# Performance work log

Measured on AMD Instinct MI355X. Metric: run time of the kernel, lower is better.

Reference implementation:

```python
import jax, jax.numpy as jnp
import numpy as np
from jax import lax

DIM = 256
NUM_HEADS = 8
SW = 7
HEAD_DIM = DIM // NUM_HEADS
SCALE = HEAD_DIM ** -0.5


def setup_inputs() -> dict:
    key = jax.random.key(0)
    ks = jax.random.split(key, 7)
    B, C, H, W = 8, DIM, 56, 56
    x = jax.random.normal(ks[0], (B, C, H, W), dtype=jnp.float32)
    w_qkv = jax.random.normal(ks[1], (3 * C, C), dtype=jnp.float32) * 0.02
    b_qkv = jnp.zeros((3 * C,), dtype=jnp.float32)
    # depthwise 3x3 kernel, OIHW with feature_group_count=C -> (C,1,3,3)
    w_dw = jax.random.normal(ks[2], (C, 1, 3, 3), dtype=jnp.float32) * 0.02
    b_dw = jnp.zeros((C,), dtype=jnp.float32)
    w_proj = jax.random.normal(ks[3], (C, C), dtype=jnp.float32) * 0.02
    b_proj = jnp.zeros((C,), dtype=jnp.float32)
    return {"x": x, "w_qkv": w_qkv, "b_qkv": b_qkv, "w_dw": w_dw,
            "b_dw": b_dw, "w_proj": w_proj, "b_proj": b_proj}


def _conv1x1(x, w, b):
    # x:[B,C,H,W], w:[O,C] -> [B,O,H,W]
    return jnp.einsum('bchw,oc->bohw', x, w) + b[None, :, None, None]


def _dwconv3x3(x, w, b):
    C = x.shape[1]
    y = lax.conv_general_dilated(x, w, window_strides=(1, 1), padding='SAME',
                                 dimension_numbers=('NCHW', 'OIHW', 'NCHW'),
                                 feature_group_count=C)
    return y + b[None, :, None, None]


def _stripe_attn_H(q, k, v, sw):
    # q,k,v: [B,h,C,H,W]; local attention within sw-thick horizontal stripes
    B, h, C, H, W = q.shape
    sw = min(sw, H)
    pad = (-H) % sw
    if pad:
        pw = [(0, 0)] * 3 + [(0, pad), (0, 0)]
        q = jnp.pad(q, pw); k = jnp.pad(k, pw); v = jnp.pad(v, pw)
    Hp = H + pad
    n = Hp // sw

    def rs(t):
        # -> [B,h,n, sw*W, C]
        return t.reshape(B, h, C, n, sw, W).transpose(0, 1, 3, 4, 5, 2).reshape(B, h, n, sw * W, C)

    qs, ks_, vs = rs(q) * SCALE, rs(k), rs(v)
    attn = jax.nn.softmax(jnp.einsum('bhnqc,bhnkc->bhnqk', qs, ks_), axis=-1)
    out = jnp.einsum('bhnqk,bhnkc->bhnqc', attn, vs)
    out = out.reshape(B, h, n, sw, W, C).transpose(0, 1, 5, 2, 3, 4).reshape(B, h, C, Hp, W)
    return out[:, :, :, :H, :]


def _stripe_attn_W(q, k, v, sw):
    # attention within sw-thick vertical stripes; softmax is permutation-
    # equivariant over the stripe sequence, so transposing H<->W and reusing
    # the H-stripe kernel computes identical math.
    t = lambda a: a.transpose(0, 1, 2, 4, 3)
    return t(_stripe_attn_H(t(q), t(k), t(v), sw))


def reference(x, w_qkv, b_qkv, w_dw, b_dw, w_proj, b_proj):
    B, C, H, W = x.shape
    hh = NUM_HEADS // 2
    qkv = _conv1x1(x, w_qkv, b_qkv)
    q, k, v = jnp.split(qkv, 3, axis=1)
    v = v + _dwconv3x3(v, w_dw, b_dw)

    def heads(t):
        return t.reshape(B, NUM_HEADS, HEAD_DIM, H, W)

    q, k, v = heads(q), heads(k), heads(v)
    out_h = _stripe_attn_H(q[:, :hh], k[:, :hh], v[:, :hh], SW)
    out_w = _stripe_attn_W(q[:, hh:], k[:, hh:], v[:, hh:], SW)
    out = jnp.concatenate([out_h, out_w], axis=1).reshape(B, C, H, W)
    return _conv1x1(out, w_proj, b_proj)
```

## Files before the change

### kernel.cpp

```cpp
#include <hip/hip_runtime.h>
#include <hip/hip_bf16.h>
#include <stdint.h>

#define Bn 8
#define Cn 256
#define Hn 56
#define Wn 56
#define HWn 3136
#define NHEADS 8
#define HDIM 32
#define SEQ 392
#define NSTR 8
#define QKV_LD 768
#define KSC (0.17677669529663689f * 1.4426950408889634f)

#if __has_builtin(__builtin_amdgcn_exp2f)
#define EXP2(x) __builtin_amdgcn_exp2f(x)
#else
#define EXP2(x) exp2f(x)
#endif

typedef short short8 __attribute__((ext_vector_type(8)));
typedef float floatx4 __attribute__((ext_vector_type(4)));

__device__ __forceinline__ unsigned short f2bf(float f) {
  union { float f; uint32_t u; } v; v.f = f;
  uint32_t u = v.u;
  u += 0x7fffu + ((u >> 16) & 1u);
  return (unsigned short)(u >> 16);
}
__device__ __forceinline__ float bf2f(unsigned short h) {
  union { uint32_t u; float f; } v; v.u = ((uint32_t)h) << 16;
  return v.f;
}
__device__ __forceinline__ uint32_t cvt_pk_bf16(float lo, float hi) {
  uint32_t r;
  asm("v_cvt_pk_bf16_f32 %0, %1, %2" : "=v"(r) : "v"(lo), "v"(hi));
  return r;
}
__device__ __forceinline__ void gload16(const unsigned short* g, unsigned short* l) {
  __builtin_amdgcn_global_load_lds((const __attribute__((address_space(1))) void*)g,
                                   (__attribute__((address_space(3))) void*)l, 16, 0, 0);
}

__global__ __launch_bounds__(256) void k_cvt2(const float* __restrict__ a,
                                              const float* __restrict__ b2,
                                              unsigned short* __restrict__ da,
                                              unsigned short* __restrict__ db) {
  int i = blockIdx.x * 256 + threadIdx.x;
  if (i < 49152) {
    float4 v = ((const float4*)a)[i];
    ushort4 o;
    o.x = f2bf(v.x); o.y = f2bf(v.y); o.z = f2bf(v.z); o.w = f2bf(v.w);
    ((ushort4*)da)[i] = o;
  } else {
    int k = i - 49152;
    float4 v = ((const float4*)b2)[k];
    ushort4 o;
    o.x = f2bf(v.x); o.y = f2bf(v.y); o.z = f2bf(v.z); o.w = f2bf(v.w);
    ((ushort4*)db)[k] = o;
  }
}

__global__ __launch_bounds__(256) void k_trans_x(const float* __restrict__ x,
                                                 unsigned short* __restrict__ xt) {
  __shared__ float tile[32][33];
  int pb = blockIdx.x, cb = blockIdx.y, b = blockIdx.z;
  int t = threadIdx.x;
  int c = t >> 3, p4 = (t & 7) * 4;
  float4 v = *(const float4*)(x + (((size_t)b * Cn + cb * 32 + c) * HWn + pb * 32 + p4));
  tile[c][p4 + 0] = v.x; tile[c][p4 + 1] = v.y; tile[c][p4 + 2] = v.z; tile[c][p4 + 3] = v.w;
  __syncthreads();
  int p = t >> 3, c4 = (t & 7) * 4;
  ushort4 o;
  o.x = f2bf(tile[c4 + 0][p]); o.y = f2bf(tile[c4 + 1][p]);
  o.z = f2bf(tile[c4 + 2][p]); o.w = f2bf(tile[c4 + 3][p]);
  *(ushort4*)(xt + (((size_t)b * HWn + pb * 32 + p) * Cn + cb * 32 + c4)) = o;
}

template <int EPI>
__global__ __launch_bounds__(512) void k_gemm(const unsigned short* __restrict__ A,
                                              const unsigned short* __restrict__ Bt,
                                              const float* __restrict__ bias,
                                              unsigned short* __restrict__ outB,
                                              float* __restrict__ outF,
                                              int M, int N, int K, int nm, int nper) {
  __shared__ __align__(16) char SH[EPI ? 67584 : 65536];
  unsigned short* As = (unsigned short*)SH;
  unsigned short* Bs = As + 16384;
  int t = threadIdx.x;
  int raw = blockIdx.x;
  int chunk = gridDim.x >> 3;
  int wg = (raw & 7) * chunk + (raw >> 3);
  int b = wg / nper, r = wg % nper;
  int m0 = (r % nm) * 128, n0 = (r / nm) * 128;
  const unsigned short* Bb = Bt + (size_t)b * N * K;
  int lane = t & 63, w = t >> 6;
  int wr = w >> 1, wc = w & 1;
  int g = lane >> 4, q = lane & 15;
  int srow8 = lane >> 3;
  int slot = lane & 7;

  const unsigned short* Ag[2];
  const unsigned short* Bg[2];
  bool bok[2];
  int ldst[2];
#pragma unroll
  for (int i = 0; i < 2; i++) {
    int row = i * 64 + w * 8 + srow8;
    int cs = slot ^ srow8;
    Ag[i] = A + (size_t)(m0 + row) * K + cs * 8;
    int nr = n0 + row;
    bok[i] = (nr < N);
    Bg[i] = Bb + (size_t)(bok[i] ? nr : (N - 1)) * K + cs * 8;
    ldst[i] = (i * 64 + w * 8) * 64;
  }

  floatx4 z4 = {0.f, 0.f, 0.f, 0.f};
  floatx4 acc[2][4];
#pragma unroll
  for (int i = 0; i < 2; i++)
#pragma unroll
    for (int j = 0; j < 4; j++) acc[i][j] = z4;

#pragma unroll
  for (int i = 0; i < 2; i++) gload16(Ag[i], &As[ldst[i]]);
#pragma unroll
  for (int i = 0; i < 2; i++) if (bok[i]) gload16(Bg[i], &Bs[ldst[i]]);
  asm volatile("s_waitcnt vmcnt(0)" ::: "memory");
  __syncthreads();

  int cur = 0;
  for (int tt = 0; tt < 4; tt++) {
    if (tt < 3) {
      int k0 = (tt + 1) * 64;
      int nb = (cur ^ 1) * 8192;
#pragma unroll
      for (int i = 0; i < 2; i++) gload16(Ag[i] + k0, &As[nb + ldst[i]]);
#pragma unroll
      for (int i = 0; i < 2; i++) if (bok[i]) gload16(Bg[i] + k0, &Bs[nb + ldst[i]]);
    }
    int cb = cur * 8192;
#pragma unroll
    for (int kk = 0; kk < 64; kk += 32) {
      short8 af[2], bfr[4];
#pragma unroll
      for (int i = 0; i < 2; i++) {
        int row = wr * 32 + i * 16 + q;
        af[i] = *(const short8*)&As[cb + row * 64 + ((((kk >> 3) + g) ^ (q & 7)) << 3)];
      }
#pragma unroll
      for (int j = 0; j < 4; j++) {
        int row = wc * 64 + j * 16 + q;
        bfr[j] = *(const short8*)&Bs[cb + row * 64 + ((((kk >> 3) + g) ^ (q & 7)) << 3)];
      }
#pragma unroll
      for (int i = 0; i < 2; i++)
#pragma unroll
        for (int j = 0; j < 4; j++)
          acc[i][j] = __builtin_amdgcn_mfma_f32_16x16x32_bf16(af[i], bfr[j], acc[i][j], 0, 0, 0);
    }
    if (tt < 3) {
      asm volatile("s_waitcnt vmcnt(0)" ::: "memory");
      __syncthreads();
      cur ^= 1;
    }
  }

  __syncthreads();
  if (EPI == 0) {
    unsigned short* E = (unsigned short*)SH;
#pragma unroll
    for (int i = 0; i < 2; i++) {
      int ob = m0 + wr * 32 + i * 16 + g * 4;
      float bs0 = bias[ob + 0], bs1 = bias[ob + 1], bs2 = bias[ob + 2], bs3 = bias[ob + 3];
      float sc = (ob >= 256 && ob < 512) ? KSC : 1.0f;
      int lobg = wr * 4 + i * 2 + (g >> 1);
#pragma unroll
      for (int j = 0; j < 4; j++) {
        int lc = wc * 64 + j * 16 + q;
        ushort4 o;
        o.x = f2bf((acc[i][j][0] + bs0) * sc);
        o.y = f2bf((acc[i][j][1] + bs1) * sc);
        o.z = f2bf((acc[i][j][2] + bs2) * sc);
        o.w = f2bf((acc[i][j][3] + bs3) * sc);
        *(ushort4*)&E[lc * 128 + ((lobg ^ (lc & 7)) << 3) + (g & 1) * 4] = o;
      }
    }
    __syncthreads();
    int c = t >> 2, part = t & 3;
    int col = n0 + c;
    if (col < N) {
      unsigned short* dst = outB + ((size_t)b * N + col) * M + m0;
#pragma unroll
      for (int k2 = part * 4; k2 < part * 4 + 4; k2++) {
        short8 v = *(const short8*)&E[c * 128 + ((k2 ^ (c & 7)) << 3)];
        *(short8*)(dst + k2 * 8) = v;
      }
    }
  } else {
    float* Ef = (float*)SH;
#pragma unroll
    for (int i = 0; i < 2; i++) {
      int ob = m0 + wr * 32 + i * 16 + g * 4;
      int lob = wr * 32 + i * 16 + g * 4;
      float bs0 = bias[ob + 0], bs1 = bias[ob + 1], bs2 = bias[ob + 2], bs3 = bias[ob + 3];
#pragma unroll
      for (int j = 0; j < 4; j++) {
        int lc = wc * 64 + j * 16 + q;
        Ef[(lob + 0) * 132 + lc] = acc[i][j][0] + bs0;
        Ef[(lob + 1) * 132 + lc] = acc[i][j][1] + bs1;
        Ef[(lob + 2) * 132 + lc] = acc[i][j][2] + bs2;
        Ef[(lob + 3) * 132 + lc] = acc[i][j][3] + bs3;
      }
    }
    __syncthreads();
    int rr = t >> 2, seg = t & 3;
    float* dst = outF + (size_t)b * M * N + (size_t)(m0 + rr) * N + n0;
#pragma unroll
    for (int k2 = 0; k2 < 8; k2++) {
      int col = seg * 32 + k2 * 4;
      if (n0 + col < N) {
        floatx4 v = *(const floatx4*)&Ef[rr * 132 + col];
        *(floatx4*)(dst + col) = v;
      }
    }
  }
}

__global__ __launch_bounds__(256) void k_dwconv_t(const unsigned short* __restrict__ qkv,
                                                  const float* __restrict__ wdw,
                                                  const float* __restrict__ bdw,
                                                  unsigned short* __restrict__ vmt,
                                                  unsigned short* __restrict__ qkvw) {
  __shared__ float wS[1152];
  __shared__ float bS[128];
  __shared__ __align__(16) unsigned short tile[16][140];
  int t = threadIdx.x;
  int pass = blockIdx.y, b = blockIdx.z;
  for (int i = t; i < 1152; i += 256) wS[i] = wdw[pass * 1152 + i];
  if (t < 128) bS[t] = bdw[pass * 128 + t];

  int pi = t >> 4, c8 = (t & 15) * 8;
  int i16 = blockIdx.x * 16 + pi;
  int h, w;
  if (pass == 0) { h = i16 / Wn; w = i16 % Wn; }
  else           { w = i16 / Hn; h = i16 % Hn; }

  if (pass == 1) {
    int pi2 = t >> 4, c16 = (t & 15) * 16;
    int ib = blockIdx.x * 16 + pi2;
    int w2 = ib / Hn, h2 = ib % Hn;
    size_t src = ((size_t)b * HWn + h2 * Wn + w2) * QKV_LD;
    int sch = (c16 < 128) ? (128 + c16) : (256 + c16);
    short8 v0 = *(const short8*)(qkv + src + sch);
    short8 v1 = *(const short8*)(qkv + src + sch + 8);
    unsigned short* dst = qkvw + ((size_t)b * HWn + ib) * 256 + c16;
    *(short8*)dst = v0;
    *(short8*)(dst + 8) = v1;
  }
  __syncthreads();

  const unsigned short* vq = qkv + 512 + pass * 128 + c8;
  float a[8];
  short8 vc = *(const short8*)(vq + ((size_t)b * HWn + h * Wn + w) * QKV_LD);
#pragma unroll
  for (int e = 0; e < 8; e++) a[e] = bf2f((unsigned short)vc[e]) + bS[c8 + e];
#pragma unroll
  for (int ky = 0; ky < 3; ky++) {
    int hh = h + ky - 1;
    if (hh < 0 || hh >= Hn) continue;
#pragma unroll
    for (int kx = 0; kx < 3; kx++) {
      int ww = w + kx - 1;
      if (ww < 0 || ww >= Wn) continue;
      short8 vn = *(const short8*)(vq + ((size_t)b * HWn + hh * Wn + ww) * QKV_LD);
#pragma unroll
      for (int e = 0; e < 8; e++) a[e] += bf2f((unsigned short)vn[e]) * wS[(c8 + e) * 9 + ky * 3 + kx];
    }
  }
  short8 o;
#pragma unroll
  for (int e = 0; e < 8; e++) o[e] = (short)f2bf(a[e]);
  *(short8*)&tile[pi][c8] = o;
  __syncthreads();

  int dd = t >> 1, half = t & 1;
  short8 ov;
#pragma unroll
  for (int k2 = 0; k2 < 8; k2++) ov[k2] = (short)tile[half * 8 + k2][dd];
  *(short8*)(vmt + ((size_t)(b * Cn + pass * 128 + dd)) * HWn + blockIdx.x * 16 + half * 8) = ov;
}

__global__ __launch_bounds__(512) void k_attn(const unsigned short* __restrict__ qkv,
                                              const unsigned short* __restrict__ qkvw,
                                              const unsigned short* __restrict__ vmt,
                                              unsigned short* __restrict__ aout) {
  __shared__ __align__(16) unsigned short Ks[12288];
  __shared__ __align__(16) unsigned short Vf[12800];
  __shared__ __align__(16) unsigned short Pf[4096];
  int s = blockIdx.x;
  int hd = blockIdx.y & 7, b = blockIdx.y >> 3;
  int t = threadIdx.x, lane = t & 63, wv = t >> 6;
  bool wst = (hd >= 4);
  int q = lane & 15, g = lane >> 4;
  int sbase = s * SEQ;

  const unsigned short* base; int ld, qoff, koff;
  if (wst) { base = qkvw + (size_t)b * HWn * 256;    ld = 256;    qoff = (hd - 4) * 32; koff = 128 + (hd - 4) * 32; }
  else     { base = qkv  + (size_t)b * HWn * QKV_LD; ld = QKV_LD; qoff = hd * 32;       koff = 256 + hd * 32; }

  short8 qpre[4];
#pragma unroll
  for (int it = 0; it < 4; it++) {
    int qb = it * 8 + wv;
    int qi = qb * 16 + q;
    int qil = (qi < SEQ) ? qi : 391;
    qpre[it] = *(const short8*)(base + qoff + (size_t)(sbase + qil) * ld + g * 8);
  }

  const unsigned short* kgp = base + koff;
#pragma unroll
  for (int P = 0; P < 3; P++) {
    int key = P * 128 + (t >> 2);
    int gg = t & 3;
    short8 kv = *(const short8*)(kgp + (size_t)(sbase + key) * ld + gg * 8);
    *(short8*)&Ks[((((key >> 4) * 4 + gg) * 16) + (key & 15)) * 8] = kv;
  }
  short8 kf24;
  {
    int key = 384 + q; if (key > 391) key = 391;
    kf24 = *(const short8*)(kgp + (size_t)(sbase + key) * ld + g * 8);
  }
  const unsigned short* vg = vmt + ((size_t)(b * Cn + hd * HDIM)) * HWn + sbase;
  for (int idx = t; idx < 1600; idx += 512) {
    int d = idx / 50, Gc = idx % 50;
    short8 vv = *(const short8*)(vg + (size_t)d * HWn + Gc * 8);
    *(short8*)&Vf[(Gc * 32 + (d ^ (Gc & 7))) * 8] = vv;
  }
  __syncthreads();

  floatx4 z4 = {0.f, 0.f, 0.f, 0.f};
  unsigned short* Pw = &Pf[wv * 512];
  int gh = g >> 1, ge = (g & 1) * 4;

#pragma unroll
  for (int it = 0; it < 4; it++) {
    int qb = it * 8 + wv;
    if (qb >= 25) continue;
    int qi = qb * 16 + q;
    int qil = (qi < SEQ) ? qi : 391;
    short8 qf = qpre[it];

    floatx4 sacc[25];
#pragma unroll
    for (int j = 0; j < 24; j++) {
      short8 kf = *(const short8*)&Ks[((j * 4 + g) * 16 + q) * 8];
      sacc[j] = __builtin_amdgcn_mfma_f32_16x16x32_bf16(kf, qf, z4, 0, 0, 0);
    }
    sacc[24] = __builtin_amdgcn_mfma_f32_16x16x32_bf16(kf24, qf, z4, 0, 0, 0);
    if (g >= 2) { sacc[24][0] = sacc[24][1] = sacc[24][2] = sacc[24][3] = -3.0e38f; }

    float sm = 0.f;
#pragma unroll
    for (int j = 0; j < 25; j++) {
      float e0 = EXP2(sacc[j][0]); float e1 = EXP2(sacc[j][1]);
      float e2 = EXP2(sacc[j][2]); float e3 = EXP2(sacc[j][3]);
      sacc[j][0] = e0; sacc[j][1] = e1; sacc[j][2] = e2; sacc[j][3] = e3;
      sm += (e0 + e1) + (e2 + e3);
    }
    sm += __shfl_xor(sm, 16);
    sm += __shfl_xor(sm, 32);
    float rcp = 1.0f / sm;

#define WRITEP(cc) do {                                                        \
    enum { jbW = (2*(cc)+1 < 25) ? (2*(cc)+1) : 24 };                          \
    uint2 wA, wB;                                                              \
    wA.x = cvt_pk_bf16(sacc[2*(cc)][0], sacc[2*(cc)][1]);                      \
    wA.y = cvt_pk_bf16(sacc[2*(cc)][2], sacc[2*(cc)][3]);                      \
    if (2*(cc)+1 < 25) {                                                       \
      wB.x = cvt_pk_bf16(sacc[jbW][0], sacc[jbW][1]);                          \
      wB.y = cvt_pk_bf16(sacc[jbW][2], sacc[jbW][3]);                          \
    } else { wB.x = 0u; wB.y = 0u; }                                           \
    *(uint2*)&Pw[(gh * 16 + q) * 8 + ge] = wA;                                 \
    *(uint2*)&Pw[((2 + gh) * 16 + q) * 8 + ge] = wB;                           \
  } while (0)

    floatx4 o0 = z4, o1 = z4;
    WRITEP(0);
#pragma unroll
    for (int ch = 0; ch < 13; ch++) {
      asm volatile("s_waitcnt lgkmcnt(0)" ::: "memory");
      short8 pfr = *(const short8*)&Pw[(g * 16 + q) * 8];
      int Gc = ch * 4 + g; if (Gc > 49) Gc = 49;
      int sw = Gc & 7;
      short8 vf0 = *(const short8*)&Vf[(Gc * 32 + (q ^ sw)) * 8];
      short8 vf1 = *(const short8*)&Vf[(Gc * 32 + 16 + (q ^ sw)) * 8];
      if (ch < 12) {
        switch (ch + 1) {
          case 1: WRITEP(1); break;  case 2: WRITEP(2); break;
          case 3: WRITEP(3); break;  case 4: WRITEP(4); break;
          case 5: WRITEP(5); break;  case 6: WRITEP(6); break;
          case 7: WRITEP(7); break;  case 8: WRITEP(8); break;
          case 9: WRITEP(9); break;  case 10: WRITEP(10); break;
          case 11: WRITEP(11); break; case 12: WRITEP(12); break;
        }
      }
      o0 = __builtin_amdgcn_mfma_f32_16x16x32_bf16(vf0, pfr, o0, 0, 0, 0);
      o1 = __builtin_amdgcn_mfma_f32_16x16x32_bf16(vf1, pfr, o1, 0, 0, 0);
    }
#undef WRITEP

    if (qi < SEQ) {
      int pq = wst ? ((qil % Wn) * Wn + s * 7 + qil / Wn) : (sbase + qil);
      size_t ob = ((size_t)b * HWn + pq) * Cn + hd * HDIM;
      ushort4 u0, u1;
      u0.x = f2bf(o0[0] * rcp); u0.y = f2bf(o0[1] * rcp);
      u0.z = f2bf(o0[2] * rcp); u0.w = f2bf(o0[3] * rcp);
      u1.x = f2bf(o1[0] * rcp); u1.y = f2bf(o1[1] * rcp);
      u1.z = f2bf(o1[2] * rcp); u1.w = f2bf(o1[3] * rcp);
      *(ushort4*)(aout + ob + g * 4) = u0;
      *(ushort4*)(aout + ob + 16 + g * 4) = u1;
    }
  }
}

extern "C" void kernel_launch(void* const* d_in, const int* in_sizes, int n_in,
                              void* d_out, int out_size, void* d_ws, size_t ws_size,
                              hipStream_t stream) {
  const float* x     = (const float*)d_in[0];
  const float* wqkv  = (const float*)d_in[1];
  const float* bqkv  = (const float*)d_in[2];
  const float* wdw   = (const float*)d_in[3];
  const float* bdw   = (const float*)d_in[4];
  const float* wproj = (const float*)d_in[5];
  const float* bproj = (const float*)d_in[6];
  float* out = (float*)d_out;

  unsigned short* xt   = (unsigned short*)d_ws;
  unsigned short* wqb  = xt + (size_t)Bn * HWn * Cn;
  unsigned short* wpb  = wqb + 768 * 256;
  unsigned short* qkvb = wpb + 256 * 256;
  unsigned short* vmt  = qkvb + (size_t)Bn * HWn * QKV_LD;
  unsigned short* aout = vmt + (size_t)Bn * HWn * Cn;
  unsigned short* qkvw = aout + (size_t)Bn * HWn * Cn;

  k_cvt2<<<dim3(256), 256, 0, stream>>>(wqkv, wproj, wqb, wpb);
  k_trans_x<<<dim3(98, 8, Bn), 256, 0, stream>>>(x, xt);
  k_gemm<0><<<dim3(1200), 512, 0, stream>>>(wqb, xt, bqkv, qkvb, nullptr, 768, HWn, 256, 6, 150);
  k_dwconv_t<<<dim3(196, 2, Bn), 256, 0, stream>>>(qkvb, wdw, bdw, vmt, qkvw);
  k_attn<<<dim3(NSTR, Bn * NHEADS), 512, 0, stream>>>(qkvb, qkvw, vmt, aout);
  k_gemm<1><<<dim3(400), 512, 0, stream>>>(wpb, aout, bproj, nullptr, out, 256, HWn, 256, 2, 50);
}
```

Baseline: 114.1 us.

## Scatter Q/K into per-head stripe-ordered buffers from QKV GEMM epilogue

```diff
diff --git a/kernel.cpp b/kernel.cpp
--- a/kernel.cpp
+++ b/kernel.cpp
@@ -84,6 +84,7 @@
                                               const float* __restrict__ bias,
                                               unsigned short* __restrict__ outB,
                                               float* __restrict__ outF,
+                                              unsigned short* __restrict__ outV,
                                               int M, int N, int K, int nm, int nper) {
   __shared__ __align__(16) char SH[EPI ? 67584 : 65536];
   unsigned short* As = (unsigned short*)SH;
@@ -191,11 +192,20 @@
     int c = t >> 2, part = t & 3;
     int col = n0 + c;
     if (col < N) {
-      unsigned short* dst = outB + ((size_t)b * N + col) * M + m0;
+      int mt = m0 >> 7;
+      unsigned short* dst;
+      if (mt < 4) {
+        int hd = (mt & 1) * 4 + part;
+        int sl = (mt >> 1) * 8 + hd;
+        int p_ord = (hd >= 4) ? ((col % Wn) * Wn + col / Wn) : col;
+        dst = outB + (((size_t)b * 16 + sl) * HWn + p_ord) * 32;
+      } else {
+        dst = outV + ((size_t)b * HWn + col) * 256 + (m0 - 512) + part * 32;
+      }
 #pragma unroll
       for (int k2 = part * 4; k2 < part * 4 + 4; k2++) {
         short8 v = *(const short8*)&E[c * 128 + ((k2 ^ (c & 7)) << 3)];
-        *(short8*)(dst + k2 * 8) = v;
+        *(short8*)(dst + (k2 - part * 4) * 8) = v;
       }
     }
   } else {
@@ -228,11 +238,10 @@
   }
 }
 
-__global__ __launch_bounds__(256) void k_dwconv_t(const unsigned short* __restrict__ qkv,
+__global__ __launch_bounds__(256) void k_dwconv_t(const unsigned short* __restrict__ vb,
                                                   const float* __restrict__ wdw,
                                                   const float* __restrict__ bdw,
-                                                  unsigned short* __restrict__ vmt,
-                                                  unsigned short* __restrict__ qkvw) {
+                                                  unsigned short* __restrict__ vmt) {
   __shared__ float wS[1152];
   __shared__ float bS[128];
   __shared__ __align__(16) unsigned short tile[16][140];
@@ -240,6 +249,7 @@
   int pass = blockIdx.y, b = blockIdx.z;
   for (int i = t; i < 1152; i += 256) wS[i] = wdw[pass * 1152 + i];
   if (t < 128) bS[t] = bdw[pass * 128 + t];
+  __syncthreads();
 
   int pi = t >> 4, c8 = (t & 15) * 8;
   int i16 = blockIdx.x * 16 + pi;
@@ -247,23 +257,9 @@
   if (pass == 0) { h = i16 / Wn; w = i16 % Wn; }
   else           { w = i16 / Hn; h = i16 % Hn; }
 
-  if (pass == 1) {
-    int pi2 = t >> 4, c16 = (t & 15) * 16;
-    int ib = blockIdx.x * 16 + pi2;
-    int w2 = ib / Hn, h2 = ib % Hn;
-    size_t src = ((size_t)b * HWn + h2 * Wn + w2) * QKV_LD;
-    int sch = (c16 < 128) ? (128 + c16) : (256 + c16);
-    short8 v0 = *(const short8*)(qkv + src + sch);
-    short8 v1 = *(const short8*)(qkv + src + sch + 8);
-    unsigned short* dst = qkvw + ((size_t)b * HWn + ib) * 256 + c16;
-    *(short8*)dst = v0;
-    *(short8*)(dst + 8) = v1;
-  }
-  __syncthreads();
-
-  const unsigned short* vq = qkv + 512 + pass * 128 + c8;
+  const unsigned short* vq = vb + pass * 128 + c8;
   float a[8];
-  short8 vc = *(const short8*)(vq + ((size_t)b * HWn + h * Wn + w) * QKV_LD);
+  short8 vc = *(const short8*)(vq + ((size_t)b * HWn + h * Wn + w) * 256);
 #pragma unroll
   for (int e = 0; e < 8; e++) a[e] = bf2f((unsigned short)vc[e]) + bS[c8 + e];
 #pragma unroll
@@ -274,7 +270,7 @@
     for (int kx = 0; kx < 3; kx++) {
       int ww = w + kx - 1;
       if (ww < 0 || ww >= Wn) continue;
-      short8 vn = *(const short8*)(vq + ((size_t)b * HWn + hh * Wn + ww) * QKV_LD);
+      short8 vn = *(const short8*)(vq + ((size_t)b * HWn + hh * Wn + ww) * 256);
 #pragma unroll
       for (int e = 0; e < 8; e++) a[e] += bf2f((unsigned short)vn[e]) * wS[(c8 + e) * 9 + ky * 3 + kx];
     }
@@ -292,8 +288,7 @@
   *(short8*)(vmt + ((size_t)(b * Cn + pass * 128 + dd)) * HWn + blockIdx.x * 16 + half * 8) = ov;
 }
 
-__global__ __launch_bounds__(512) void k_attn(const unsigned short* __restrict__ qkv,
-                                              const unsigned short* __restrict__ qkvw,
+__global__ __launch_bounds__(512) void k_attn(const unsigned short* __restrict__ qkh,
                                               const unsigned short* __restrict__ vmt,
                                               unsigned short* __restrict__ aout) {
   __shared__ __align__(16) unsigned short Ks[12288];
@@ -306,9 +301,8 @@
   int q = lane & 15, g = lane >> 4;
   int sbase = s * SEQ;
 
-  const unsigned short* base; int ld, qoff, koff;
-  if (wst) { base = qkvw + (size_t)b * HWn * 256;    ld = 256;    qoff = (hd - 4) * 32; koff = 128 + (hd - 4) * 32; }
-  else     { base = qkv  + (size_t)b * HWn * QKV_LD; ld = QKV_LD; qoff = hd * 32;       koff = 256 + hd * 32; }
+  const unsigned short* qh = qkh + (((size_t)b * 16 + hd) * HWn + sbase) * 32;
+  const unsigned short* kh = qkh + (((size_t)b * 16 + 8 + hd) * HWn + sbase) * 32;
 
   short8 qpre[4];
 #pragma unroll
@@ -316,21 +310,20 @@
     int qb = it * 8 + wv;
     int qi = qb * 16 + q;
     int qil = (qi < SEQ) ? qi : 391;
-    qpre[it] = *(const short8*)(base + qoff + (size_t)(sbase + qil) * ld + g * 8);
-  }
-
-  const unsigned short* kgp = base + koff;
+    qpre[it] = *(const short8*)(qh + (size_t)qil * 32 + g * 8);
+  }
+
 #pragma unroll
   for (int P = 0; P < 3; P++) {
     int key = P * 128 + (t >> 2);
     int gg = t & 3;
-    short8 kv = *(const short8*)(kgp + (size_t)(sbase + key) * ld + gg * 8);
+    short8 kv = *(const short8*)(kh + (size_t)key * 32 + gg * 8);
     *(short8*)&Ks[((((key >> 4) * 4 + gg) * 16) + (key & 15)) * 8] = kv;
   }
   short8 kf24;
   {
     int key = 384 + q; if (key > 391) key = 391;
-    kf24 = *(const short8*)(kgp + (size_t)(sbase + key) * ld + g * 8);
+    kf24 = *(const short8*)(kh + (size_t)key * 32 + g * 8);
   }
   const unsigned short* vg = vmt + ((size_t)(b * Cn + hd * HDIM)) * HWn + sbase;
   for (int idx = t; idx < 1600; idx += 512) {
@@ -440,15 +433,15 @@
   unsigned short* xt   = (unsigned short*)d_ws;
   unsigned short* wqb  = xt + (size_t)Bn * HWn * Cn;
   unsigned short* wpb  = wqb + 768 * 256;
-  unsigned short* qkvb = wpb + 256 * 256;
-  unsigned short* vmt  = qkvb + (size_t)Bn * HWn * QKV_LD;
+  unsigned short* qkh  = wpb + 256 * 256;
+  unsigned short* vb   = qkh + (size_t)Bn * 16 * HWn * 32;
+  unsigned short* vmt  = vb + (size_t)Bn * HWn * Cn;
   unsigned short* aout = vmt + (size_t)Bn * HWn * Cn;
-  unsigned short* qkvw = aout + (size_t)Bn * HWn * Cn;
 
   k_cvt2<<<dim3(256), 256, 0, stream>>>(wqkv, wproj, wqb, wpb);
   k_trans_x<<<dim3(98, 8, Bn), 256, 0, stream>>>(x, xt);
-  k_gemm<0><<<dim3(1200), 512, 0, stream>>>(wqb, xt, bqkv, qkvb, nullptr, 768, HWn, 256, 6, 150);
-  k_dwconv_t<<<dim3(196, 2, Bn), 256, 0, stream>>>(qkvb, wdw, bdw, vmt, qkvw);
-  k_attn<<<dim3(NSTR, Bn * NHEADS), 512, 0, stream>>>(qkvb, qkvw, vmt, aout);
-  k_gemm<1><<<dim3(400), 512, 0, stream>>>(wpb, aout, bproj, nullptr, out, 256, HWn, 256, 2, 50);
-}
+  k_gemm<0><<<dim3(1200), 512, 0, stream>>>(wqb, xt, bqkv, qkh, nullptr, vb, 768, HWn, 256, 6, 150);
+  k_dwconv_t<<<dim3(196, 2, Bn), 256, 0, stream>>>(vb, wdw, bdw, vmt);
+  k_attn<<<dim3(NSTR, Bn * NHEADS), 512, 0, stream>>>(qkh, vmt, aout);
+  k_gemm<1><<<dim3(400), 512, 0, stream>>>(wpb, aout, bproj, nullptr, out, nullptr, 256, HWn, 256, 2, 50);
+}
```

Measured after the change: 108.5 us. -4.9%, faster.
